# Kernel tuning notes

Measured on AMD Instinct MI355X. Metric: run time of the kernel, lower is better.

The kernel has to match this reference:

```python
import jax, jax.numpy as jnp
import numpy as np

D_MODEL = 1024
NUM_HEADS = 16
HEAD_DIM = D_MODEL // NUM_HEADS


def setup_inputs() -> dict:
    key = jax.random.key(0)
    ks = jax.random.split(key, 11)
    B, S, D = 2, 2048, D_MODEL
    s = 1.0 / np.sqrt(D)
    return {
        "query": jax.random.normal(ks[0], (B, S, D), jnp.float32),
        "key": jax.random.normal(ks[1], (B, S, D), jnp.float32),
        "value": jax.random.normal(ks[2], (B, S, D), jnp.float32),
        "W_q": jax.random.normal(ks[3], (D, D), jnp.float32) * s,
        "b_q": jnp.zeros((D,), jnp.float32),
        "W_k": jax.random.normal(ks[4], (D, D), jnp.float32) * s,
        "b_k": jnp.zeros((D,), jnp.float32),
        "W_v": jax.random.normal(ks[5], (D, D), jnp.float32) * s,
        "b_v": jnp.zeros((D,), jnp.float32),
        "W_o": jax.random.normal(ks[6], (D, D), jnp.float32) * s,
        "b_o": jnp.zeros((D,), jnp.float32),
    }


def reference(query, key, value, W_q, b_q, W_k, b_k, W_v, b_v, W_o, b_o):
    B, S, D = query.shape
    H, Dh = NUM_HEADS, HEAD_DIM
    # linear projections then split heads: [B, S, D] -> [B, H, S, Dh]
    def split_heads(x):
        return x.reshape(B, -1, H, Dh).transpose(0, 2, 1, 3)
    Q = split_heads(query @ W_q.T + b_q)
    K = split_heads(key @ W_k.T + b_k)
    V = split_heads(value @ W_v.T + b_v)
    # NOTE: original scales by d_model**-0.5, not head_dim**-0.5
    scale = jnp.asarray(D, Q.dtype) ** -0.5
    scores = jnp.einsum("bhqd,bhkd->bhqk", Q, K) * scale
    attn = jax.nn.softmax(scores, axis=-1)  # includes max-subtraction stabilization
    out = jnp.einsum("bhqk,bhkd->bhqd", attn, V)
    out = out.transpose(0, 2, 1, 3).reshape(B, -1, D)
    return out @ W_o.T + b_o
```

## Files before the change

kernel.cpp:

```cpp
#include <hip/hip_runtime.h>
#include <stdint.h>


typedef unsigned short u16;
typedef short s16x8 __attribute__((ext_vector_type(8)));
typedef short s16x4 __attribute__((ext_vector_type(4)));
typedef float f32x4 __attribute__((ext_vector_type(4)));
typedef u16 u16x4 __attribute__((ext_vector_type(4)));

#define S_LEN 2048
#define DMODEL 1024
#define LOG2E 1.44269504088896340736f

__device__ __forceinline__ u16 f2bf(float f) {
  union { float f; uint32_t u; } v; v.f = f;
  return (u16)((v.u + 0x8000u) >> 16);
}

__device__ __forceinline__ s16x8 ld8f(const float* s) {
  f32x4 a = *(const f32x4*)s;
  f32x4 b = *(const f32x4*)(s + 4);
  s16x8 r;
  r[0] = (short)f2bf(a[0]); r[1] = (short)f2bf(a[1]);
  r[2] = (short)f2bf(a[2]); r[3] = (short)f2bf(a[3]);
  r[4] = (short)f2bf(b[0]); r[5] = (short)f2bf(b[1]);
  r[6] = (short)f2bf(b[2]); r[7] = (short)f2bf(b[3]);
  return r;
}

struct CvtBatch { const float* s[4]; u16* d[4]; };

__global__ __launch_bounds__(256) void cvt_w(CvtBatch p) {
  const int z = blockIdx.y;
  const size_t i = ((size_t)blockIdx.x * 256 + threadIdx.x) * 8;
  *(s16x8*)(p.d[z] + i) = ld8f(p.s[z] + i);
}

#define LDA 40
struct GemmBatch {
  const void* A[3]; const u16* W[3]; const float* Bv[3]; void* C[3];
};

template <bool A_F32>
__global__ __launch_bounds__(256) void gemm_bt(GemmBatch p, int M, int N, int K) {
  __shared__ u16 As[128 * LDA];
  __shared__ u16 Ws[128 * LDA];
  const int z = blockIdx.z;
  const u16* __restrict__ W      = p.W[z];
  const float* __restrict__ bias = p.Bv[z];

  const int tid = threadIdx.x;
  const int wave = tid >> 6, lane = tid & 63;
  const int quad = lane >> 4, l16 = lane & 15;
  const int bm = blockIdx.y * 128, bn = blockIdx.x * 128;
  const int wr = (wave >> 1) * 64, wc = (wave & 1) * 64;
  const int srow = wave * 16 + (lane >> 2);
  const int skof = (lane & 3) * 8;

  f32x4 acc[4][4];
#pragma unroll
  for (int i = 0; i < 4; i++)
#pragma unroll
    for (int j = 0; j < 4; j++) acc[i][j] = {0.f, 0.f, 0.f, 0.f};

  const u16*   Wb = W + (size_t)bn * K;
  const float* Af = A_F32 ? ((const float*)p.A[z] + (size_t)bm * K) : nullptr;
  const u16*   Ah = A_F32 ? nullptr : ((const u16*)p.A[z] + (size_t)bm * K);

  s16x8 va0, va1, vw0, vw1;
  if (A_F32) {
    va0 = ld8f(Af + (size_t)(srow)      * K + skof);
    va1 = ld8f(Af + (size_t)(64 + srow) * K + skof);
  } else {
    va0 = *(const s16x8*)(Ah + (size_t)(srow)      * K + skof);
    va1 = *(const s16x8*)(Ah + (size_t)(64 + srow) * K + skof);
  }
  vw0 = *(const s16x8*)(Wb + (size_t)(srow)      * K + skof);
  vw1 = *(const s16x8*)(Wb + (size_t)(64 + srow) * K + skof);

  for (int kt = 0; kt < K; kt += 32) {
    __syncthreads();
    *(s16x8*)&As[(srow)      * LDA + skof] = va0;
    *(s16x8*)&As[(64 + srow) * LDA + skof] = va1;
    *(s16x8*)&Ws[(srow)      * LDA + skof] = vw0;
    *(s16x8*)&Ws[(64 + srow) * LDA + skof] = vw1;
    __syncthreads();

    if (kt + 32 < K) {
      const int k2 = kt + 32;
      if (A_F32) {
        va0 = ld8f(Af + (size_t)(srow)      * K + k2 + skof);
        va1 = ld8f(Af + (size_t)(64 + srow) * K + k2 + skof);
      } else {
        va0 = *(const s16x8*)(Ah + (size_t)(srow)      * K + k2 + skof);
        va1 = *(const s16x8*)(Ah + (size_t)(64 + srow) * K + k2 + skof);
      }
      vw0 = *(const s16x8*)(Wb + (size_t)(srow)      * K + k2 + skof);
      vw1 = *(const s16x8*)(Wb + (size_t)(64 + srow) * K + k2 + skof);
    }

    s16x8 a[4], b[4];
#pragma unroll
    for (int t = 0; t < 4; t++)
      a[t] = *(const s16x8*)&As[(wr + t * 16 + l16) * LDA + quad * 8];
#pragma unroll
    for (int t = 0; t < 4; t++)
      b[t] = *(const s16x8*)&Ws[(wc + t * 16 + l16) * LDA + quad * 8];
#pragma unroll
    for (int i = 0; i < 4; i++)
#pragma unroll
      for (int j = 0; j < 4; j++)
        acc[i][j] = __builtin_amdgcn_mfma_f32_16x16x32_bf16(a[i], b[j], acc[i][j], 0, 0, 0);
  }

#pragma unroll
  for (int j = 0; j < 4; j++) {
    const int col = bn + wc + j * 16 + l16;
    const float bv = bias[col];
#pragma unroll
    for (int i = 0; i < 4; i++) {
      const int row0 = bm + wr + i * 16 + quad * 4;
#pragma unroll
      for (int r = 0; r < 4; r++) {
        const float val = acc[i][j][r] + bv;
        if (A_F32)
          ((u16*)p.C[z])[(size_t)(row0 + r) * N + col] = f2bf(val);
        else
          ((float*)p.C[z])[(size_t)(row0 + r) * N + col] = val;
      }
    }
  }
}

__global__ __launch_bounds__(256) void transpose_v(const u16* __restrict__ Vp,
                                                   u16* __restrict__ Vt) {
  __shared__ u16 t[64 * 72];
  const int tid = threadIdx.x;
  const int bh = blockIdx.y, b = bh >> 4, h = bh & 15;
  const int s0 = blockIdx.x * 64;
  const int r = tid >> 4, c4 = (tid & 15) * 4;
#pragma unroll
  for (int i = 0; i < 4; i++) {
    const int s = i * 16 + r;
    u16x4 v = *(const u16x4*)&Vp[(size_t)(b * S_LEN + s0 + s) * DMODEL + h * 64 + c4];
    *(u16x4*)&t[s * 72 + c4] = v;
  }
  __syncthreads();
#pragma unroll
  for (int i = 0; i < 4; i++) {
    const int d = i * 16 + r;
    u16x4 v;
    v.x = t[(c4 + 0) * 72 + d];
    v.y = t[(c4 + 1) * 72 + d];
    v.z = t[(c4 + 2) * 72 + d];
    v.w = t[(c4 + 3) * 72 + d];
    *(u16x4*)&Vt[(size_t)(bh * 64 + d) * S_LEN + s0 + c4] = v;
  }
}

__global__ __launch_bounds__(256, 2) void attn_kernel(const u16* __restrict__ Qp,
                                                      const u16* __restrict__ Kp,
                                                      const u16* __restrict__ Vt,
                                                      u16* __restrict__ AO) {
  __shared__ u16 Qs[128 * 64];
  __shared__ u16 Ks[128 * 64];
  __shared__ u16 Vs[64 * 128];

  const int tid = threadIdx.x;
  const int wave = tid >> 6, lane = tid & 63;
  const int quad = lane >> 4, l16 = lane & 15;
  const int bh = blockIdx.y, b = bh >> 4, h = bh & 15;
  const int s0 = blockIdx.x * 128;
  const float c = 0.03125f * LOG2E;

  const int qr = lane >> 3, qc = lane & 7;
  const int vd = lane >> 4, vc = lane & 15;

#pragma unroll
  for (int i = 0; i < 4; i++) {
    const int rr = i * 32 + wave * 8 + qr;
    s16x8 qv = *(const s16x8*)(Qp + (size_t)(b * S_LEN + s0 + rr) * DMODEL + h * 64 + qc * 8);
    *(s16x8*)&Qs[rr * 64 + ((qc ^ qr) << 3)] = qv;
  }
  __syncthreads();

  s16x8 aq[2][2];
#pragma unroll
  for (int ks = 0; ks < 2; ks++)
#pragma unroll
    for (int rt = 0; rt < 2; rt++) {
      const int row = wave * 32 + rt * 16 + l16;
      const int ch = ks * 4 + quad;
      aq[ks][rt] = *(const s16x8*)&Qs[row * 64 + ((ch ^ (l16 & 7)) << 3)];
    }

  s16x8 kv[4], vv[4];
#pragma unroll
  for (int i = 0; i < 4; i++) {
    const int rr = i * 32 + wave * 8 + qr;
    kv[i] = *(const s16x8*)(Kp + (size_t)(b * S_LEN + rr) * DMODEL + h * 64 + qc * 8);
  }
#pragma unroll
  for (int i = 0; i < 4; i++) {
    const int dd = i * 16 + wave * 4 + vd;
    vv[i] = *(const s16x8*)(Vt + (size_t)(bh * 64 + dd) * S_LEN + vc * 8);
  }

  f32x4 o[2][4];
  float l_r[2] = {0.f, 0.f};
#pragma unroll
  for (int rt = 0; rt < 2; rt++)
#pragma unroll
    for (int dt = 0; dt < 4; dt++) o[rt][dt] = {0.f, 0.f, 0.f, 0.f};

  const f32x4 zf = {0.f, 0.f, 0.f, 0.f};

  for (int kt = 0; kt < S_LEN; kt += 128) {
    __syncthreads();
#pragma unroll
    for (int i = 0; i < 4; i++) {
      const int rr = i * 32 + wave * 8 + qr;
      *(s16x8*)&Ks[rr * 64 + ((qc ^ qr) << 3)] = kv[i];
    }
#pragma unroll
    for (int i = 0; i < 4; i++) {
      const int dd = i * 16 + wave * 4 + vd;
      *(s16x8*)&Vs[dd * 128 + ((vc ^ (dd & 15)) << 3)] = vv[i];
    }
    __syncthreads();

    if (kt + 128 < S_LEN) {
      const int k2 = kt + 128;
#pragma unroll
      for (int i = 0; i < 4; i++) {
        const int rr = i * 32 + wave * 8 + qr;
        kv[i] = *(const s16x8*)(Kp + (size_t)(b * S_LEN + k2 + rr) * DMODEL + h * 64 + qc * 8);
      }
#pragma unroll
      for (int i = 0; i < 4; i++) {
        const int dd = i * 16 + wave * 4 + vd;
        vv[i] = *(const s16x8*)(Vt + (size_t)(bh * 64 + dd) * S_LEN + k2 + vc * 8);
      }
    }

#pragma unroll
    for (int kvt = 0; kvt < 8; kvt++) {
      const int krow = kvt * 16 + l16;
      s16x8 ak0 = *(const s16x8*)&Ks[krow * 64 + (((0 + quad) ^ (l16 & 7)) << 3)];
      s16x8 ak1 = *(const s16x8*)&Ks[krow * 64 + (((4 + quad) ^ (l16 & 7)) << 3)];
      f32x4 sA, sB;
      sA = __builtin_amdgcn_mfma_f32_16x16x32_bf16(ak0, aq[0][0], zf, 0, 0, 0);
      sA = __builtin_amdgcn_mfma_f32_16x16x32_bf16(ak1, aq[1][0], sA, 0, 0, 0);
      sB = __builtin_amdgcn_mfma_f32_16x16x32_bf16(ak0, aq[0][1], zf, 0, 0, 0);
      sB = __builtin_amdgcn_mfma_f32_16x16x32_bf16(ak1, aq[1][1], sB, 0, 0, 0);

      s16x4 pf0, pf1;
      float rs0 = 0.f, rs1 = 0.f;
#pragma unroll
      for (int r = 0; r < 4; r++) {
        const float p0 = exp2f(sA[r] * c);
        const float p1 = exp2f(sB[r] * c);
        rs0 += p0; rs1 += p1;
        pf0[r] = (short)f2bf(p0);
        pf1[r] = (short)f2bf(p1);
      }
      l_r[0] += rs0; l_r[1] += rs1;

      const int ch = kvt * 2 + (quad >> 1);
#pragma unroll
      for (int dt = 0; dt < 4; dt++) {
        const int row = dt * 16 + l16;
        s16x4 bv = *(const s16x4*)&Vs[row * 128 + ((ch ^ l16) << 3) + (quad & 1) * 4];
        o[0][dt] = __builtin_amdgcn_mfma_f32_16x16x16bf16_1k(pf0, bv, o[0][dt], 0, 0, 0);
        o[1][dt] = __builtin_amdgcn_mfma_f32_16x16x16bf16_1k(pf1, bv, o[1][dt], 0, 0, 0);
      }
    }
  }

#pragma unroll
  for (int rt = 0; rt < 2; rt++) {
    l_r[rt] += __shfl_xor(l_r[rt], 16);
    l_r[rt] += __shfl_xor(l_r[rt], 32);
  }
#pragma unroll
  for (int rt = 0; rt < 2; rt++) {
#pragma unroll
    for (int r = 0; r < 4; r++) {
      const float linv = 1.f / __shfl(l_r[rt], quad * 4 + r);
      const int row = s0 + wave * 32 + rt * 16 + quad * 4 + r;
#pragma unroll
      for (int dt = 0; dt < 4; dt++)
        AO[(size_t)(b * S_LEN + row) * DMODEL + h * 64 + dt * 16 + l16] =
            f2bf(o[rt][dt][r] * linv);
    }
  }
}

extern "C" void kernel_launch(void* const* d_in, const int* in_sizes, int n_in,
                              void* d_out, int out_size, void* d_ws, size_t ws_size,
                              hipStream_t stream) {
  const float* query = (const float*)d_in[0];
  const float* key_  = (const float*)d_in[1];
  const float* value = (const float*)d_in[2];
  const float* W_q = (const float*)d_in[3];
  const float* b_q = (const float*)d_in[4];
  const float* W_k = (const float*)d_in[5];
  const float* b_k = (const float*)d_in[6];
  const float* W_v = (const float*)d_in[7];
  const float* b_v = (const float*)d_in[8];
  const float* W_o = (const float*)d_in[9];
  const float* b_o = (const float*)d_in[10];
  float* out = (float*)d_out;

  const int M = 2 * S_LEN;
  const int N = DMODEL, K = DMODEL;
  const size_t WSZ = (size_t)DMODEL * DMODEL;
  const size_t SZ  = (size_t)M * DMODEL;

  u16* Wqb = (u16*)d_ws;
  u16* Wkb = Wqb + WSZ;
  u16* Wvb = Wkb + WSZ;
  u16* Wob = Wvb + WSZ;
  u16* Qp  = Wob + WSZ;
  u16* Kp  = Qp + SZ;
  u16* Vp  = Kp + SZ;
  u16* Vt  = Vp + SZ;
  u16* AO  = Qp;

  CvtBatch cw;
  cw.s[0] = W_q; cw.s[1] = W_k; cw.s[2] = W_v; cw.s[3] = W_o;
  cw.d[0] = Wqb; cw.d[1] = Wkb; cw.d[2] = Wvb; cw.d[3] = Wob;
  cvt_w<<<dim3((int)(WSZ / 2048), 4), 256, 0, stream>>>(cw);

  GemmBatch p1;
  p1.A[0] = query; p1.W[0] = Wqb; p1.Bv[0] = b_q; p1.C[0] = Qp;
  p1.A[1] = key_;  p1.W[1] = Wkb; p1.Bv[1] = b_k; p1.C[1] = Kp;
  p1.A[2] = value; p1.W[2] = Wvb; p1.Bv[2] = b_v; p1.C[2] = Vp;
  gemm_bt<true><<<dim3(N / 128, M / 128, 3), 256, 0, stream>>>(p1, M, N, K);

  transpose_v<<<dim3(S_LEN / 64, 32), 256, 0, stream>>>(Vp, Vt);

  attn_kernel<<<dim3(S_LEN / 128, 32), 256, 0, stream>>>(Qp, Kp, Vt, AO);

  GemmBatch p2;
  p2.A[0] = AO; p2.W[0] = Wob; p2.Bv[0] = b_o; p2.C[0] = out;
  p2.A[1] = AO; p2.W[1] = Wob; p2.Bv[1] = b_o; p2.C[1] = out;
  p2.A[2] = AO; p2.W[2] = Wob; p2.Bv[2] = b_o; p2.C[2] = out;
  gemm_bt<false><<<dim3(N / 128, M / 128, 1), 256, 0, stream>>>(p2, M, N, K);
}
```

Measured before the change: 261.6 us.

## Pre-convert activations to bf16 and load GEMM tiles via direct global-to-LDS

```diff
diff --git a/kernel.cpp b/kernel.cpp
--- a/kernel.cpp
+++ b/kernel.cpp
@@ -28,24 +28,31 @@
   return r;
 }
 
-struct CvtBatch { const float* s[4]; u16* d[4]; };
-
-__global__ __launch_bounds__(256) void cvt_w(CvtBatch p) {
+__device__ __forceinline__ void gl2lds16(const u16* g, u16* l) {
+  __builtin_amdgcn_global_load_lds(
+      (const __attribute__((address_space(1))) uint32_t*)g,
+      (__attribute__((address_space(3))) uint32_t*)l, 16, 0, 0);
+}
+
+struct Cvt7 { const float* s[7]; u16* d[7]; int n[7]; };
+
+__global__ __launch_bounds__(256) void cvt7(Cvt7 p) {
   const int z = blockIdx.y;
-  const size_t i = ((size_t)blockIdx.x * 256 + threadIdx.x) * 8;
-  *(s16x8*)(p.d[z] + i) = ld8f(p.s[z] + i);
-}
-
-#define LDA 40
+  const int idx = blockIdx.x * 256 + threadIdx.x;
+  if (idx * 8 < p.n[z])
+    *(s16x8*)(p.d[z] + (size_t)idx * 8) = ld8f(p.s[z] + (size_t)idx * 8);
+}
+
 struct GemmBatch {
-  const void* A[3]; const u16* W[3]; const float* Bv[3]; void* C[3];
+  const u16* A[3]; const u16* W[3]; const float* Bv[3]; void* C[3];
 };
 
-template <bool A_F32>
+template <bool OUT_F32>
 __global__ __launch_bounds__(256) void gemm_bt(GemmBatch p, int M, int N, int K) {
-  __shared__ u16 As[128 * LDA];
-  __shared__ u16 Ws[128 * LDA];
+  __shared__ u16 As[128 * 64];
+  __shared__ u16 Ws[128 * 64];
   const int z = blockIdx.z;
+  const u16* __restrict__ A      = p.A[z];
   const u16* __restrict__ W      = p.W[z];
   const float* __restrict__ bias = p.Bv[z];
 
@@ -54,8 +61,9 @@
   const int quad = lane >> 4, l16 = lane & 15;
   const int bm = blockIdx.y * 128, bn = blockIdx.x * 128;
   const int wr = (wave >> 1) * 64, wc = (wave & 1) * 64;
-  const int srow = wave * 16 + (lane >> 2);
-  const int skof = (lane & 3) * 8;
+  const int sr8 = lane >> 3;
+  const int slc = (lane & 7) ^ sr8;
+  const int srow = wave * 8 + sr8;
 
   f32x4 acc[4][4];
 #pragma unroll
@@ -63,54 +71,37 @@
 #pragma unroll
     for (int j = 0; j < 4; j++) acc[i][j] = {0.f, 0.f, 0.f, 0.f};
 
-  const u16*   Wb = W + (size_t)bn * K;
-  const float* Af = A_F32 ? ((const float*)p.A[z] + (size_t)bm * K) : nullptr;
-  const u16*   Ah = A_F32 ? nullptr : ((const u16*)p.A[z] + (size_t)bm * K);
-
-  s16x8 va0, va1, vw0, vw1;
-  if (A_F32) {
-    va0 = ld8f(Af + (size_t)(srow)      * K + skof);
-    va1 = ld8f(Af + (size_t)(64 + srow) * K + skof);
-  } else {
-    va0 = *(const s16x8*)(Ah + (size_t)(srow)      * K + skof);
-    va1 = *(const s16x8*)(Ah + (size_t)(64 + srow) * K + skof);
-  }
-  vw0 = *(const s16x8*)(Wb + (size_t)(srow)      * K + skof);
-  vw1 = *(const s16x8*)(Wb + (size_t)(64 + srow) * K + skof);
-
-  for (int kt = 0; kt < K; kt += 32) {
+  const u16* Ab = A + (size_t)bm * K;
+  const u16* Wb = W + (size_t)bn * K;
+
+  for (int kt = 0; kt < K; kt += 64) {
     __syncthreads();
-    *(s16x8*)&As[(srow)      * LDA + skof] = va0;
-    *(s16x8*)&As[(64 + srow) * LDA + skof] = va1;
-    *(s16x8*)&Ws[(srow)      * LDA + skof] = vw0;
-    *(s16x8*)&Ws[(64 + srow) * LDA + skof] = vw1;
+#pragma unroll
+    for (int i = 0; i < 4; i++)
+      gl2lds16(Ab + (size_t)(i * 32 + srow) * K + kt + slc * 8,
+               &As[(i * 32 + wave * 8) * 64]);
+#pragma unroll
+    for (int i = 0; i < 4; i++)
+      gl2lds16(Wb + (size_t)(i * 32 + srow) * K + kt + slc * 8,
+               &Ws[(i * 32 + wave * 8) * 64]);
     __syncthreads();
 
-    if (kt + 32 < K) {
-      const int k2 = kt + 32;
-      if (A_F32) {
-        va0 = ld8f(Af + (size_t)(srow)      * K + k2 + skof);
-        va1 = ld8f(Af + (size_t)(64 + srow) * K + k2 + skof);
-      } else {
-        va0 = *(const s16x8*)(Ah + (size_t)(srow)      * K + k2 + skof);
-        va1 = *(const s16x8*)(Ah + (size_t)(64 + srow) * K + k2 + skof);
-      }
-      vw0 = *(const s16x8*)(Wb + (size_t)(srow)      * K + k2 + skof);
-      vw1 = *(const s16x8*)(Wb + (size_t)(64 + srow) * K + k2 + skof);
-    }
-
-    s16x8 a[4], b[4];
-#pragma unroll
-    for (int t = 0; t < 4; t++)
-      a[t] = *(const s16x8*)&As[(wr + t * 16 + l16) * LDA + quad * 8];
-#pragma unroll
-    for (int t = 0; t < 4; t++)
-      b[t] = *(const s16x8*)&Ws[(wc + t * 16 + l16) * LDA + quad * 8];
-#pragma unroll
-    for (int i = 0; i < 4; i++)
-#pragma unroll
-      for (int j = 0; j < 4; j++)
-        acc[i][j] = __builtin_amdgcn_mfma_f32_16x16x32_bf16(a[i], b[j], acc[i][j], 0, 0, 0);
+#pragma unroll
+    for (int ks = 0; ks < 2; ks++) {
+      const int ch = ks * 4 + quad;
+      s16x8 a[4], b[4];
+#pragma unroll
+      for (int t = 0; t < 4; t++)
+        a[t] = *(const s16x8*)&As[(wr + t * 16 + l16) * 64 + ((ch ^ (l16 & 7)) << 3)];
+#pragma unroll
+      for (int t = 0; t < 4; t++)
+        b[t] = *(const s16x8*)&Ws[(wc + t * 16 + l16) * 64 + ((ch ^ (l16 & 7)) << 3)];
+#pragma unroll
+      for (int i = 0; i < 4; i++)
+#pragma unroll
+        for (int j = 0; j < 4; j++)
+          acc[i][j] = __builtin_amdgcn_mfma_f32_16x16x32_bf16(a[i], b[j], acc[i][j], 0, 0, 0);
+    }
   }
 
 #pragma unroll
@@ -123,10 +114,10 @@
 #pragma unroll
       for (int r = 0; r < 4; r++) {
         const float val = acc[i][j][r] + bv;
-        if (A_F32)
+        if (OUT_F32)
+          ((float*)p.C[z])[(size_t)(row0 + r) * N + col] = val;
+        else
           ((u16*)p.C[z])[(size_t)(row0 + r) * N + col] = f2bf(val);
-        else
-          ((float*)p.C[z])[(size_t)(row0 + r) * N + col] = val;
       }
     }
   }
@@ -321,22 +312,30 @@
   u16* Wkb = Wqb + WSZ;
   u16* Wvb = Wkb + WSZ;
   u16* Wob = Wvb + WSZ;
-  u16* Qp  = Wob + WSZ;
+  u16* Qa  = Wob + WSZ;
+  u16* Ka  = Qa + SZ;
+  u16* Va  = Ka + SZ;
+  u16* Qp  = Va + SZ;
   u16* Kp  = Qp + SZ;
   u16* Vp  = Kp + SZ;
-  u16* Vt  = Vp + SZ;
+  u16* Vt  = Qa;
   u16* AO  = Qp;
 
-  CvtBatch cw;
-  cw.s[0] = W_q; cw.s[1] = W_k; cw.s[2] = W_v; cw.s[3] = W_o;
-  cw.d[0] = Wqb; cw.d[1] = Wkb; cw.d[2] = Wvb; cw.d[3] = Wob;
-  cvt_w<<<dim3((int)(WSZ / 2048), 4), 256, 0, stream>>>(cw);
+  Cvt7 cw;
+  cw.s[0] = W_q;   cw.d[0] = Wqb; cw.n[0] = (int)WSZ;
+  cw.s[1] = W_k;   cw.d[1] = Wkb; cw.n[1] = (int)WSZ;
+  cw.s[2] = W_v;   cw.d[2] = Wvb; cw.n[2] = (int)WSZ;
+  cw.s[3] = W_o;   cw.d[3] = Wob; cw.n[3] = (int)WSZ;
+  cw.s[4] = query; cw.d[4] = Qa;  cw.n[4] = (int)SZ;
+  cw.s[5] = key_;  cw.d[5] = Ka;  cw.n[5] = (int)SZ;
+  cw.s[6] = value; cw.d[6] = Va;  cw.n[6] = (int)SZ;
+  cvt7<<<dim3((int)(SZ / 2048), 7), 256, 0, stream>>>(cw);
 
   GemmBatch p1;
-  p1.A[0] = query; p1.W[0] = Wqb; p1.Bv[0] = b_q; p1.C[0] = Qp;
-  p1.A[1] = key_;  p1.W[1] = Wkb; p1.Bv[1] = b_k; p1.C[1] = Kp;
-  p1.A[2] = value; p1.W[2] = Wvb; p1.Bv[2] = b_v; p1.C[2] = Vp;
-  gemm_bt<true><<<dim3(N / 128, M / 128, 3), 256, 0, stream>>>(p1, M, N, K);
+  p1.A[0] = Qa; p1.W[0] = Wqb; p1.Bv[0] = b_q; p1.C[0] = Qp;
+  p1.A[1] = Ka; p1.W[1] = Wkb; p1.Bv[1] = b_k; p1.C[1] = Kp;
+  p1.A[2] = Va; p1.W[2] = Wvb; p1.Bv[2] = b_v; p1.C[2] = Vp;
+  gemm_bt<false><<<dim3(N / 128, M / 128, 3), 256, 0, stream>>>(p1, M, N, K);
 
   transpose_v<<<dim3(S_LEN / 64, 32), 256, 0, stream>>>(Vp, Vt);
 
@@ -346,5 +345,5 @@
   p2.A[0] = AO; p2.W[0] = Wob; p2.Bv[0] = b_o; p2.C[0] = out;
   p2.A[1] = AO; p2.W[1] = Wob; p2.Bv[1] = b_o; p2.C[1] = out;
   p2.A[2] = AO; p2.W[2] = Wob; p2.Bv[2] = b_o; p2.C[2] = out;
-  gemm_bt<false><<<dim3(N / 128, M / 128, 1), 256, 0, stream>>>(p2, M, N, K);
-}
+  gemm_bt<true><<<dim3(N / 128, M / 128, 1), 256, 0, stream>>>(p2, M, N, K);
+}
```

After: 259.1 us. No clear change (-0.9%).
